# Performance work log

Measured on AMD Instinct MI355X. Metric: run time of the kernel, lower is better.

The kernel has to match this reference:

```python
import jax, jax.numpy as jnp
import numpy as np

B, L, E, H = 2, 2048, 1024, 16
D = E // H  # 64


def setup_inputs() -> dict:
    key = jax.random.key(0)
    ks = jax.random.split(key, 9)
    return {
        "query": jax.random.normal(ks[0], (B, L, E), dtype=jnp.float32),
        "value": jax.random.normal(ks[1], (B, L, E), dtype=jnp.float32),
        "key": jax.random.normal(ks[2], (B, L, E), dtype=jnp.float32),
        "mask": jax.random.randint(ks[3], (B, 1, L, L), 0, 2, dtype=jnp.int32),
        "Wq": jax.random.normal(ks[4], (D, D), dtype=jnp.float32) * 0.05,
        "Wk": jax.random.normal(ks[5], (D, D), dtype=jnp.float32) * 0.05,
        "Wv": jax.random.normal(ks[6], (D, D), dtype=jnp.float32) * 0.05,
        "Wfc": jax.random.normal(ks[7], (E, E), dtype=jnp.float32) * 0.02,
        "bfc": jax.random.normal(ks[8], (E,), dtype=jnp.float32) * 0.02,
    }


def reference(query, value, key, mask, Wq, Wk, Wv, Wfc, bfc):
    b, q_len, _ = query.shape
    k_len = key.shape[1]
    v_len = value.shape[1]
    # split heads: [b, l, H, D]
    q = query.reshape(b, q_len, H, D)
    k = key.reshape(b, k_len, H, D)
    v = value.reshape(b, v_len, H, D)
    # per-head linear projections (shared weights across heads, no bias)
    q = jnp.einsum('bqhd,ed->bqhe', q, Wq)
    k = jnp.einsum('bkhd,ed->bkhe', k, Wk)
    v = jnp.einsum('bvhd,ed->bvhe', v, Wv)
    # attention scores [b, H, q, k]
    attn = jnp.einsum('bqhd,bkhd->bhqk', q, k)
    # NOTE: original masks BEFORE scaling, and scales by sqrt(embedding_size)
    attn = jnp.where(mask == 0, jnp.float32(-1e20), attn)
    attn = attn / jnp.float32(E ** 0.5)
    attn = jax.nn.softmax(attn, axis=3)
    out = jnp.einsum('bhqk,bkhd->bqhd', attn, v).reshape(b, q_len, E)
    out = out @ Wfc.T + bfc
    return out
```

## Files before the change

### kernel.cpp

```cpp
#include <hip/hip_runtime.h>
#include <hip/hip_bf16.h>


#define B_ 2
#define L_ 2048
#define E_ 1024
#define H_ 16
#define D_ 64

typedef __attribute__((ext_vector_type(8))) short s8v;
typedef __attribute__((ext_vector_type(4))) float f4v;
typedef __attribute__((ext_vector_type(2))) float f2v;

__device__ __forceinline__ f4v mfma16(s8v a, s8v b, f4v c) {
    return __builtin_amdgcn_mfma_f32_16x16x32_bf16(a, b, c, 0, 0, 0);
}

__device__ __forceinline__ float fast_exp2(float x) {
    return __builtin_amdgcn_exp2f(x);
}

__device__ __forceinline__ ushort bf16bits(float f) {
    __hip_bfloat16 h = __float2bfloat16(f);
    return *(ushort*)&h;
}

__device__ __forceinline__ void glds16(const __hip_bfloat16* g, ushort* l) {
    __builtin_amdgcn_global_load_lds(
        (const __attribute__((address_space(1))) void*)g,
        (__attribute__((address_space(3))) void*)l,
        16, 0, 0);
}

__device__ __forceinline__ s8v ld8_dual(const void* p, size_t idx, bool isf32) {
    if (isf32) {
        const float* pf = (const float*)p + idx;
        f4v f0 = *(const f4v*)pf;
        f4v f1 = *(const f4v*)(pf + 4);
        s8v r;
        r[0] = (short)bf16bits(f0[0]); r[1] = (short)bf16bits(f0[1]);
        r[2] = (short)bf16bits(f0[2]); r[3] = (short)bf16bits(f0[3]);
        r[4] = (short)bf16bits(f1[0]); r[5] = (short)bf16bits(f1[1]);
        r[6] = (short)bf16bits(f1[2]); r[7] = (short)bf16bits(f1[3]);
        return r;
    }
    return *(const s8v*)((const __hip_bfloat16*)p + idx);
}

__device__ __forceinline__ s8v ld8_ws(const __hip_bfloat16* p) {
    return *(const s8v*)p;
}

__device__ __forceinline__ s8v u4_to_s8(uint a, uint b, uint c, uint d) {
    union { uint u[4]; s8v v; } x;
    x.u[0] = a; x.u[1] = b; x.u[2] = c; x.u[3] = d;
    return x.v;
}

__device__ __forceinline__ bool block_detect_f32(const void* q_in, int* sflag) {
    if (threadIdx.x == 0) *sflag = 0;
    __syncthreads();
    const ushort* qq = (const ushort*)q_in + (threadIdx.x & 255) * 16;
    int bad = 0;
    #pragma unroll
    for (int i = 0; i < 16; ++i) bad += (((qq[i] >> 7) & 0xFF) >= 0x8E);
    bad += __shfl_xor(bad, 1);
    bad += __shfl_xor(bad, 2);
    bad += __shfl_xor(bad, 4);
    bad += __shfl_xor(bad, 8);
    bad += __shfl_xor(bad, 16);
    bad += __shfl_xor(bad, 32);
    if ((threadIdx.x & 63) == 0 && threadIdx.x < 256) atomicAdd(sflag, bad);
    __syncthreads();
    return *sflag > 100;
}

__device__ __forceinline__ void cvt_piece(
    size_t i4, const void* Wfc, const void* bfc,
    __hip_bfloat16* wfc_bf, __hip_bfloat16* bfc_bf, bool isf32)
{
    const size_t base = i4 * 4;
    const size_t n1 = (size_t)E_ * E_;
    if (base >= n1 + E_) return;
    const void* src = (base < n1) ? Wfc : bfc;
    const size_t off = (base < n1) ? base : base - n1;
    __hip_bfloat16* dst = (base < n1) ? (wfc_bf + off) : (bfc_bf + off);
    if (isf32) {
        f4v v = *(const f4v*)((const float*)src + off);
        #pragma unroll
        for (int j = 0; j < 4; ++j) dst[j] = __float2bfloat16(v[j]);
    } else {
        *(ushort4*)dst = *(const ushort4*)((const ushort*)src + off);
    }
}

__global__ __launch_bounds__(256) void proj_all_kernel(
    const void* __restrict__ q_in, const void* __restrict__ k_in,
    const void* __restrict__ v_in,
    const void* __restrict__ Wq, const void* __restrict__ Wk,
    const void* __restrict__ Wv,
    const void* __restrict__ Wfc, const void* __restrict__ bfc,
    const int* __restrict__ mask, unsigned long long* __restrict__ mbits,
    __hip_bfloat16* __restrict__ qp, __hip_bfloat16* __restrict__ kp,
    __hip_bfloat16* __restrict__ vpT,
    __hip_bfloat16* __restrict__ wfc_bf, __hip_bfloat16* __restrict__ bfc_bf)
{
    __shared__ __align__(16) ushort tile[64][72];
    __shared__ __align__(16) ushort wlds[64 * 72];
    __shared__ int sflag;
    const int wave = threadIdx.x >> 6;
    const int lane = threadIdx.x & 63;
    const int quad = lane >> 4;
    const int l16  = lane & 15;

    if (blockIdx.y == 3) {
        const int lane_ = threadIdx.x & 63;
        const size_t wbase = (size_t)blockIdx.x * 128 + wave * 32;
        #pragma unroll 4
        for (int i = 0; i < 32; ++i) {
            const size_t widx = wbase + i;
            const int v = mask[widx * 64 + lane_];
            const unsigned long long bal = __ballot(v != 0);
            if (lane_ == 0) mbits[widx] = bal;
        }
        return;
    }

    const bool isf32 = block_detect_f32(q_in, &sflag);

    if (blockIdx.y == 4) {
        cvt_piece((size_t)blockIdx.x * 256 + threadIdx.x, Wfc, bfc, wfc_bf, bfc_bf, isf32);
        if (blockIdx.x == 0)
            cvt_piece((size_t)(E_ * (size_t)E_ / 4) + threadIdx.x, Wfc, bfc, wfc_bf, bfc_bf, isf32);
        return;
    }

    {
        const void* W = blockIdx.y == 0 ? Wq : (blockIdx.y == 1 ? Wk : Wv);
        const int row = threadIdx.x >> 2;
        const int c0  = (threadIdx.x & 3) * 16;
        if (isf32) {
            const float* wsrc = (const float*)W + row * 64 + c0;
            #pragma unroll
            for (int j = 0; j < 16; ++j)
                wlds[row * 72 + c0 + j] = bf16bits(wsrc[j]);
        } else {
            const ushort* wsrc = (const ushort*)W + row * 64 + c0;
            *(s8v*)&wlds[row * 72 + c0]     = *(const s8v*)wsrc;
            *(s8v*)&wlds[row * 72 + c0 + 8] = *(const s8v*)(wsrc + 8);
        }
    }
    __syncthreads();

    if (blockIdx.y < 2) {
        const void* X = blockIdx.y == 0 ? q_in : k_in;
        __hip_bfloat16* dst = blockIdx.y == 0 ? qp : kp;
        const float oscale = (blockIdx.y == 0) ? 0.045084439755930314f : 1.0f;
        const int m0 = (blockIdx.x * 4 + wave) * 16;

        const size_t abase = (size_t)(m0 + l16) * D_;
        s8v a0 = ld8_dual(X, abase + quad * 8, isf32);
        s8v a1 = ld8_dual(X, abase + 32 + quad * 8, isf32);

        f4v acc[4];
        #pragma unroll
        for (int nt = 0; nt < 4; ++nt) {
            const ushort* wr = &wlds[(nt * 16 + l16) * 72];
            s8v b0 = *(const s8v*)(wr + quad * 8);
            s8v b1 = *(const s8v*)(wr + 32 + quad * 8);
            f4v c = {0.f, 0.f, 0.f, 0.f};
            c = mfma16(a0, b0, c);
            c = mfma16(a1, b1, c);
            acc[nt] = c;
        }
        #pragma unroll
        for (int r = 0; r < 4; ++r) {
            const int m = m0 + quad * 4 + r;
            #pragma unroll
            for (int nt = 0; nt < 4; ++nt) {
                const int e = nt * 16 + l16;
                dst[(size_t)m * D_ + e] = __float2bfloat16(acc[nt][r] * oscale);
            }
        }
    } else {
        const int l0 = (blockIdx.x & 31) * 64;
        const int bh = blockIdx.x >> 5;
        const int b = bh >> 4, h = bh & 15;
        const int lw = l0 + wave * 16;

        const size_t xbase = ((size_t)(b * L_ + lw + l16)) * E_ + h * D_;
        s8v a0 = ld8_dual(v_in, xbase + quad * 8, isf32);
        s8v a1 = ld8_dual(v_in, xbase + 32 + quad * 8, isf32);

        #pragma unroll
        for (int nt = 0; nt < 4; ++nt) {
            const int e = nt * 16 + l16;
            const ushort* wr = &wlds[e * 72];
            s8v b0 = *(const s8v*)(wr + quad * 8);
            s8v b1 = *(const s8v*)(wr + 32 + quad * 8);
            f4v c = {0.f, 0.f, 0.f, 0.f};
            c = mfma16(a0, b0, c);
            c = mfma16(a1, b1, c);
            #pragma unroll
            for (int r = 0; r < 4; ++r)
                tile[wave * 16 + quad * 4 + r][e] = bf16bits(c[r]);
        }
        __syncthreads();
        const int e  = threadIdx.x >> 2;
        const int lc = (threadIdx.x & 3) * 16;
        s8v s0, s1;
        #pragma unroll
        for (int i = 0; i < 8; ++i) {
            s0[i] = (short)tile[lc + i][e];
            s1[i] = (short)tile[lc + 8 + i][e];
        }
        __hip_bfloat16* drow = vpT + ((size_t)bh * D_ + e) * L_ + l0 + lc;
        *(s8v*)drow = s0;
        *(s8v*)(drow + 8) = s1;
    }
}

__global__ __launch_bounds__(256) void cvt_wfc_kernel(
    const void* __restrict__ Wfc, const void* __restrict__ bfc,
    __hip_bfloat16* __restrict__ wfc_bf, __hip_bfloat16* __restrict__ bfc_bf,
    const void* __restrict__ q_in)
{
    __shared__ int sflag;
    const bool isf32 = block_detect_f32(q_in, &sflag);
    cvt_piece((size_t)blockIdx.x * 256 + threadIdx.x, Wfc, bfc, wfc_bf, bfc_bf, isf32);
}

__global__ __launch_bounds__(256, 4) void attn_kernel(
    const __hip_bfloat16* __restrict__ qp,
    const __hip_bfloat16* __restrict__ kp,
    const __hip_bfloat16* __restrict__ vpT,
    const unsigned long long* __restrict__ mbits,
    __hip_bfloat16* __restrict__ attn_out)
{
    __shared__ __align__(16) ushort kbuf[2][64 * 64];
    __shared__ __align__(16) ushort vbuf[2][64 * 64];

    const int wave = threadIdx.x >> 6;
    const int lane = threadIdx.x & 63;
    const int quad = lane >> 4;
    const int l16  = lane & 15;
    const int sw   = l16 & 7;
    const int bh = blockIdx.y;
    const int b = bh >> 4, h = bh & 15;
    const int q0 = blockIdx.x * 64 + wave * 16;

    const __hip_bfloat16* kbh = kp + (size_t)b * L_ * E_ + h * D_;
    const __hip_bfloat16* vbh = vpT + (size_t)bh * D_ * L_;
    const unsigned long long* mrow = mbits + ((size_t)b * L_ + q0 + l16) * 32;

    const int lrow = lane >> 3;
    const int lchk = (lane & 7) ^ lrow;
    const int r0 = wave * 16;
    const __hip_bfloat16* kg0 = kbh + (size_t)(r0 + lrow) * E_ + lchk * 8;
    const __hip_bfloat16* kg1 = kbh + (size_t)(r0 + 8 + lrow) * E_ + lchk * 8;
    const __hip_bfloat16* vg0 = vbh + (size_t)(r0 + lrow) * L_ + lchk * 8;
    const __hip_bfloat16* vg1 = vbh + (size_t)(r0 + 8 + lrow) * L_ + lchk * 8;

    const __hip_bfloat16* qbase = qp + (size_t)b * L_ * E_ + h * D_ + (size_t)q0 * E_;
    s8v qa0 = ld8_ws(qbase + (size_t)l16 * E_ + quad * 8);
    s8v qa1 = ld8_ws(qbase + (size_t)l16 * E_ + 32 + quad * 8);

    f2v rs2 = {0.f, 0.f};
    f4v o[4];
    #pragma unroll
    for (int nt = 0; nt < 4; ++nt) o[nt] = (f4v){0.f, 0.f, 0.f, 0.f};

    glds16(kg0, &kbuf[0][r0 * 64]);
    glds16(kg1, &kbuf[0][r0 * 64 + 512]);
    glds16(vg0, &vbuf[0][r0 * 64]);
    glds16(vg1, &vbuf[0][r0 * 64 + 512]);
    __syncthreads();

    const int shq = quad * 4;
    int cur = 0;
    for (int it = 0; it < 32; ++it) {
        const int k0 = it * 64;
        const unsigned long long wq = mrow[it];
        const uint wlo_sh = ((uint)wq) >> shq;
        const uint whi_sh = ((uint)(wq >> 32)) >> shq;
        if (it < 31) {
            glds16(kg0 + (size_t)(k0 + 64) * E_, &kbuf[cur ^ 1][r0 * 64]);
            glds16(kg1 + (size_t)(k0 + 64) * E_, &kbuf[cur ^ 1][r0 * 64 + 512]);
            glds16(vg0 + (k0 + 64), &vbuf[cur ^ 1][r0 * 64]);
            glds16(vg1 + (k0 + 64), &vbuf[cur ^ 1][r0 * 64 + 512]);
        }
        f4v s[4];
        #pragma unroll
        for (int nt = 0; nt < 4; ++nt) {
            const ushort* kr = &kbuf[cur][(nt * 16 + l16) * 64];
            s8v kb0 = *(const s8v*)(kr + ((quad ^ sw) << 3));
            s8v kb1 = *(const s8v*)(kr + (((quad + 4) ^ sw) << 3));
            f4v c = {0.f, 0.f, 0.f, 0.f};
            c = mfma16(kb0, qa0, c);
            c = mfma16(kb1, qa1, c);
            s[nt] = c;
        }
        uint dw[4][2];
        #pragma unroll
        for (int nt = 0; nt < 4; ++nt) {
            const uint hs = (nt & 2) ? whi_sh : wlo_sh;
            float pr[4];
            #pragma unroll
            for (int r = 0; r < 4; ++r) {
                const float p = fast_exp2(s[nt][r]);
                const int m = __builtin_amdgcn_sbfe((int)hs, ((nt & 1) << 4) + r, 1);
                pr[r] = __uint_as_float(__float_as_uint(p) & (uint)m);
            }
            rs2 += (f2v){pr[0], pr[1]};
            rs2 += (f2v){pr[2], pr[3]};
            asm("v_cvt_pk_bf16_f32 %0, %1, %2"
                : "=v"(dw[nt][0]) : "v"(pr[0]), "v"(pr[1]));
            asm("v_cvt_pk_bf16_f32 %0, %1, %2"
                : "=v"(dw[nt][1]) : "v"(pr[2]), "v"(pr[3]));
        }
        uint w00 = dw[0][0], w10 = dw[1][0];
        uint w01 = dw[0][1], w11 = dw[1][1];
        uint w20 = dw[2][0], w30 = dw[3][0];
        uint w21 = dw[2][1], w31 = dw[3][1];
        asm("v_permlane32_swap_b32 %0, %1" : "+v"(w00), "+v"(w10));
        asm("v_permlane16_swap_b32 %0, %1" : "+v"(w00), "+v"(w10));
        asm("v_permlane32_swap_b32 %0, %1" : "+v"(w01), "+v"(w11));
        asm("v_permlane16_swap_b32 %0, %1" : "+v"(w01), "+v"(w11));
        asm("v_permlane32_swap_b32 %0, %1" : "+v"(w20), "+v"(w30));
        asm("v_permlane16_swap_b32 %0, %1" : "+v"(w20), "+v"(w30));
        asm("v_permlane32_swap_b32 %0, %1" : "+v"(w21), "+v"(w31));
        asm("v_permlane16_swap_b32 %0, %1" : "+v"(w21), "+v"(w31));
        s8v pa0 = u4_to_s8(w00, w01, w10, w11);
        s8v pa1 = u4_to_s8(w20, w21, w30, w31);
        #pragma unroll
        for (int nt = 0; nt < 4; ++nt) {
            const ushort* vr = &vbuf[cur][(nt * 16 + l16) * 64];
            s8v vb0 = *(const s8v*)(vr + ((quad ^ sw) << 3));
            s8v vb1 = *(const s8v*)(vr + (((quad + 4) ^ sw) << 3));
            o[nt] = mfma16(pa0, vb0, o[nt]);
            o[nt] = mfma16(pa1, vb1, o[nt]);
        }
        __syncthreads();
        cur ^= 1;
    }
    float v = rs2[0] + rs2[1];
    v += __shfl_xor(v, 16, 64);
    v += __shfl_xor(v, 32, 64);
    #pragma unroll
    for (int r = 0; r < 4; ++r) {
        const int qrow = quad * 4 + r;
        const float li = __shfl(v, qrow, 64);
        const float inv = 1.0f / fmaxf(li, 1e-30f);
        const int row = q0 + qrow;
        #pragma unroll
        for (int nt = 0; nt < 4; ++nt) {
            const int d = nt * 16 + l16;
            attn_out[((size_t)(b * L_ + row)) * E_ + h * D_ + d] =
                __float2bfloat16(o[nt][r] * inv);
        }
    }
}

__global__ __launch_bounds__(512, 2) void fc_kernel(
    const __hip_bfloat16* __restrict__ x,
    const __hip_bfloat16* __restrict__ wfc_bf,
    const __hip_bfloat16* __restrict__ bfc_bf,
    void* __restrict__ out, const void* __restrict__ q_in)
{
    __shared__ __align__(16) ushort abuf[2][128 * 64];
    __shared__ __align__(16) ushort bbuf[2][128 * 64];
    __shared__ int sflag;
    const bool isf32 = block_detect_f32(q_in, &sflag);
    const int wave = threadIdx.x >> 6;
    const int lane = threadIdx.x & 63;
    const int quad = lane >> 4;
    const int l16  = lane & 15;
    const int sw   = l16 & 7;
    const int m0 = blockIdx.x * 128;
    const int n0 = blockIdx.y * 128;
    const int wr = wave >> 2;
    const int wc = wave & 3;

    const int lrow = lane >> 3;
    const int lchk = (lane & 7) ^ lrow;

    const __hip_bfloat16* ag[2];
    const __hip_bfloat16* bg[2];
    #pragma unroll
    for (int c = 0; c < 2; ++c) {
        ag[c] = x      + (size_t)(m0 + c * 64 + wave * 8 + lrow) * E_ + lchk * 8;
        bg[c] = wfc_bf + (size_t)(n0 + c * 64 + wave * 8 + lrow) * E_ + lchk * 8;
    }

    f4v acc[4][2];
    #pragma unroll
    for (int fm = 0; fm < 4; ++fm)
        #pragma unroll
        for (int fn = 0; fn < 2; ++fn) acc[fm][fn] = (f4v){0.f, 0.f, 0.f, 0.f};

    #pragma unroll
    for (int c = 0; c < 2; ++c) {
        glds16(ag[c], &abuf[0][(c * 64 + wave * 8) * 64]);
        glds16(bg[c], &bbuf[0][(c * 64 + wave * 8) * 64]);
    }
    __syncthreads();

    int cur = 0;
    for (int it = 0; it < 16; ++it) {
        if (it < 15) {
            #pragma unroll
            for (int c = 0; c < 2; ++c) {
                glds16(ag[c] + (it + 1) * 64, &abuf[cur ^ 1][(c * 64 + wave * 8) * 64]);
                glds16(bg[c] + (it + 1) * 64, &bbuf[cur ^ 1][(c * 64 + wave * 8) * 64]);
            }
        }
        s8v a0[4], a1[4];
        #pragma unroll
        for (int fm = 0; fm < 4; ++fm) {
            const ushort* ar = &abuf[cur][(wr * 64 + fm * 16 + l16) * 64];
            a0[fm] = *(const s8v*)(ar + ((quad ^ sw) << 3));
            a1[fm] = *(const s8v*)(ar + (((quad + 4) ^ sw) << 3));
        }
        #pragma unroll
        for (int fn = 0; fn < 2; ++fn) {
            const ushort* br = &bbuf[cur][(wc * 32 + fn * 16 + l16) * 64];
            s8v b0 = *(const s8v*)(br + ((quad ^ sw) << 3));
            s8v b1 = *(const s8v*)(br + (((quad + 4) ^ sw) << 3));
            #pragma unroll
            for (int fm = 0; fm < 4; ++fm) {
                acc[fm][fn] = mfma16(a0[fm], b0, acc[fm][fn]);
                acc[fm][fn] = mfma16(a1[fm], b1, acc[fm][fn]);
            }
        }
        __syncthreads();
        cur ^= 1;
    }
    #pragma unroll
    for (int fm = 0; fm < 4; ++fm) {
        #pragma unroll
        for (int r = 0; r < 4; ++r) {
            const int m = m0 + wr * 64 + fm * 16 + quad * 4 + r;
            #pragma unroll
            for (int fn = 0; fn < 2; ++fn) {
                const int n = n0 + wc * 32 + fn * 16 + l16;
                const float val = acc[fm][fn][r] + __bfloat162float(bfc_bf[n]);
                if (isf32) ((float*)out)[(size_t)m * E_ + n] = val;
                else       ((__hip_bfloat16*)out)[(size_t)m * E_ + n] = __float2bfloat16(val);
            }
        }
    }
}

extern "C" void kernel_launch(void* const* d_in, const int* in_sizes, int n_in,
                              void* d_out, int out_size, void* d_ws, size_t ws_size,
                              hipStream_t stream) {
    const void* query = d_in[0];
    const void* value = d_in[1];
    const void* key   = d_in[2];
    const int*  mask  = (const int*)d_in[3];
    const void* Wq  = d_in[4];
    const void* Wk  = d_in[5];
    const void* Wv  = d_in[6];
    const void* Wfc = d_in[7];
    const void* bfc = d_in[8];

    char* ws = (char*)d_ws;
    unsigned long long* mbits     = (unsigned long long*)(ws + (64u << 10));
    __hip_bfloat16* qp            = (__hip_bfloat16*)(ws + (2u  << 20));
    __hip_bfloat16* kp            = (__hip_bfloat16*)(ws + (10u << 20));
    __hip_bfloat16* vpT           = (__hip_bfloat16*)(ws + (18u << 20));
    __hip_bfloat16* attn_out      = (__hip_bfloat16*)(ws + (26u << 20));

    const bool big_ws = ws_size >= (37ull << 20);
    __hip_bfloat16* wfc_bf = big_ws ? (__hip_bfloat16*)(ws + (34ull << 20)) : qp;
    __hip_bfloat16* bfc_bf = wfc_bf + (size_t)E_ * E_;

    proj_all_kernel<<<dim3(1024, big_ws ? 5 : 4), 256, 0, stream>>>(
        query, key, value, Wq, Wk, Wv, Wfc, bfc, mask, mbits,
        qp, kp, vpT, wfc_bf, bfc_bf);
    attn_kernel<<<dim3(32, 32), 256, 0, stream>>>(qp, kp, vpT, mbits, attn_out);
    if (!big_ws)
        cvt_wfc_kernel<<<1025, 256, 0, stream>>>(Wfc, bfc, wfc_bf, bfc_bf, query);
    fc_kernel<<<dim3(32, 8), 512, 0, stream>>>(attn_out, wfc_bf, bfc_bf, d_out, query);
}
```

Baseline: 221.6 us.

## Store Q/K projections head-major and shrink FC tiles to 128x64

The projection kernel now writes Q and K in a [b, h, l, d] head-major layout, so the attention kernel reads contiguous 64-element rows with stride D instead of strided rows with stride E. The FC GEMM moves from 512-thread 128x128 tiles to 256-thread 128x64 tiles with a doubled grid, aiming for more blocks in flight and better occupancy. Each FC block reloads the A tile for half as many output columns, which costs more redundant A traffic.

Measured after the change: 222.0 us. Within noise of the previous version (+0.2%).

```diff
diff --git a/kernel.cpp b/kernel.cpp
--- a/kernel.cpp
+++ b/kernel.cpp
@@ -176,10 +176,15 @@
         #pragma unroll
         for (int r = 0; r < 4; ++r) {
             const int m = m0 + quad * 4 + r;
+            const int h = m & 15;
+            const int bl = m >> 4;
+            const int b = bl >> 11;
+            const int l = bl & (L_ - 1);
             #pragma unroll
             for (int nt = 0; nt < 4; ++nt) {
                 const int e = nt * 16 + l16;
-                dst[(size_t)m * D_ + e] = __float2bfloat16(acc[nt][r] * oscale);
+                dst[(((size_t)(b * H_ + h)) * L_ + l) * D_ + e] =
+                    __float2bfloat16(acc[nt][r] * oscale);
             }
         }
     } else {
@@ -249,21 +254,21 @@
     const int b = bh >> 4, h = bh & 15;
     const int q0 = blockIdx.x * 64 + wave * 16;
 
-    const __hip_bfloat16* kbh = kp + (size_t)b * L_ * E_ + h * D_;
+    const __hip_bfloat16* kbh = kp + (size_t)bh * L_ * D_;
     const __hip_bfloat16* vbh = vpT + (size_t)bh * D_ * L_;
     const unsigned long long* mrow = mbits + ((size_t)b * L_ + q0 + l16) * 32;
 
     const int lrow = lane >> 3;
     const int lchk = (lane & 7) ^ lrow;
     const int r0 = wave * 16;
-    const __hip_bfloat16* kg0 = kbh + (size_t)(r0 + lrow) * E_ + lchk * 8;
-    const __hip_bfloat16* kg1 = kbh + (size_t)(r0 + 8 + lrow) * E_ + lchk * 8;
+    const __hip_bfloat16* kg0 = kbh + (size_t)(r0 + lrow) * D_ + lchk * 8;
+    const __hip_bfloat16* kg1 = kbh + (size_t)(r0 + 8 + lrow) * D_ + lchk * 8;
     const __hip_bfloat16* vg0 = vbh + (size_t)(r0 + lrow) * L_ + lchk * 8;
     const __hip_bfloat16* vg1 = vbh + (size_t)(r0 + 8 + lrow) * L_ + lchk * 8;
 
-    const __hip_bfloat16* qbase = qp + (size_t)b * L_ * E_ + h * D_ + (size_t)q0 * E_;
-    s8v qa0 = ld8_ws(qbase + (size_t)l16 * E_ + quad * 8);
-    s8v qa1 = ld8_ws(qbase + (size_t)l16 * E_ + 32 + quad * 8);
+    const __hip_bfloat16* qbase = qp + ((size_t)bh * L_ + q0) * D_;
+    s8v qa0 = ld8_ws(qbase + (size_t)l16 * D_ + quad * 8);
+    s8v qa1 = ld8_ws(qbase + (size_t)l16 * D_ + 32 + quad * 8);
 
     f2v rs2 = {0.f, 0.f};
     f4v o[4];
@@ -284,8 +289,8 @@
         const uint wlo_sh = ((uint)wq) >> shq;
         const uint whi_sh = ((uint)(wq >> 32)) >> shq;
         if (it < 31) {
-            glds16(kg0 + (size_t)(k0 + 64) * E_, &kbuf[cur ^ 1][r0 * 64]);
-            glds16(kg1 + (size_t)(k0 + 64) * E_, &kbuf[cur ^ 1][r0 * 64 + 512]);
+            glds16(kg0 + (size_t)(k0 + 64) * D_, &kbuf[cur ^ 1][r0 * 64]);
+            glds16(kg1 + (size_t)(k0 + 64) * D_, &kbuf[cur ^ 1][r0 * 64 + 512]);
             glds16(vg0 + (k0 + 64), &vbuf[cur ^ 1][r0 * 64]);
             glds16(vg1 + (k0 + 64), &vbuf[cur ^ 1][r0 * 64 + 512]);
         }
@@ -361,14 +366,14 @@
     }
 }
 
-__global__ __launch_bounds__(512, 2) void fc_kernel(
+__global__ __launch_bounds__(256, 4) void fc_kernel(
     const __hip_bfloat16* __restrict__ x,
     const __hip_bfloat16* __restrict__ wfc_bf,
     const __hip_bfloat16* __restrict__ bfc_bf,
     void* __restrict__ out, const void* __restrict__ q_in)
 {
     __shared__ __align__(16) ushort abuf[2][128 * 64];
-    __shared__ __align__(16) ushort bbuf[2][128 * 64];
+    __shared__ __align__(16) ushort bbuf[2][64 * 64];
     __shared__ int sflag;
     const bool isf32 = block_detect_f32(q_in, &sflag);
     const int wave = threadIdx.x >> 6;
@@ -377,20 +382,21 @@
     const int l16  = lane & 15;
     const int sw   = l16 & 7;
     const int m0 = blockIdx.x * 128;
-    const int n0 = blockIdx.y * 128;
-    const int wr = wave >> 2;
-    const int wc = wave & 3;
+    const int n0 = blockIdx.y * 64;
+    const int wr = wave >> 1;
+    const int wc = wave & 1;
 
     const int lrow = lane >> 3;
     const int lchk = (lane & 7) ^ lrow;
 
-    const __hip_bfloat16* ag[2];
+    const __hip_bfloat16* ag[4];
+    #pragma unroll
+    for (int c = 0; c < 4; ++c)
+        ag[c] = x + (size_t)(m0 + c * 32 + wave * 8 + lrow) * E_ + lchk * 8;
     const __hip_bfloat16* bg[2];
     #pragma unroll
-    for (int c = 0; c < 2; ++c) {
-        ag[c] = x      + (size_t)(m0 + c * 64 + wave * 8 + lrow) * E_ + lchk * 8;
-        bg[c] = wfc_bf + (size_t)(n0 + c * 64 + wave * 8 + lrow) * E_ + lchk * 8;
-    }
+    for (int c = 0; c < 2; ++c)
+        bg[c] = wfc_bf + (size_t)(n0 + c * 32 + wave * 8 + lrow) * E_ + lchk * 8;
 
     f4v acc[4][2];
     #pragma unroll
@@ -399,20 +405,20 @@
         for (int fn = 0; fn < 2; ++fn) acc[fm][fn] = (f4v){0.f, 0.f, 0.f, 0.f};
 
     #pragma unroll
-    for (int c = 0; c < 2; ++c) {
-        glds16(ag[c], &abuf[0][(c * 64 + wave * 8) * 64]);
-        glds16(bg[c], &bbuf[0][(c * 64 + wave * 8) * 64]);
-    }
+    for (int c = 0; c < 4; ++c) glds16(ag[c], &abuf[0][(c * 32 + wave * 8) * 64]);
+    #pragma unroll
+    for (int c = 0; c < 2; ++c) glds16(bg[c], &bbuf[0][(c * 32 + wave * 8) * 64]);
     __syncthreads();
 
     int cur = 0;
     for (int it = 0; it < 16; ++it) {
         if (it < 15) {
             #pragma unroll
-            for (int c = 0; c < 2; ++c) {
-                glds16(ag[c] + (it + 1) * 64, &abuf[cur ^ 1][(c * 64 + wave * 8) * 64]);
-                glds16(bg[c] + (it + 1) * 64, &bbuf[cur ^ 1][(c * 64 + wave * 8) * 64]);
-            }
+            for (int c = 0; c < 4; ++c)
+                glds16(ag[c] + (it + 1) * 64, &abuf[cur ^ 1][(c * 32 + wave * 8) * 64]);
+            #pragma unroll
+            for (int c = 0; c < 2; ++c)
+                glds16(bg[c] + (it + 1) * 64, &bbuf[cur ^ 1][(c * 32 + wave * 8) * 64]);
         }
         s8v a0[4], a1[4];
         #pragma unroll
@@ -481,5 +487,5 @@
     attn_kernel<<<dim3(32, 32), 256, 0, stream>>>(qp, kp, vpT, mbits, attn_out);
     if (!big_ws)
         cvt_wfc_kernel<<<1025, 256, 0, stream>>>(Wfc, bfc, wfc_bf, bfc_bf, query);
-    fc_kernel<<<dim3(32, 8), 512, 0, stream>>>(attn_out, wfc_bf, bfc_bf, d_out, query);
-}
+    fc_kernel<<<dim3(32, 16), 256, 0, stream>>>(attn_out, wfc_bf, bfc_bf, d_out, query);
+}
```
